# Kernel tuning notes

Hardware: AMD Instinct MI355X
Metric: run time of the kernel (lower is better)

The kernel has to match this reference:

```python
import jax, jax.numpy as jnp
import numpy as np
from jax import lax

EPS = 1e-5

def _conv(x, w, pad):
    # x: NCHW, w: OIHW, stride 1
    return lax.conv_general_dilated(x, w, (1, 1), [(pad, pad), (pad, pad)],
                                    dimension_numbers=('NCHW', 'OIHW', 'NCHW'))

def _binconv(x, w):
    # IR-Net/ReActNet HardBinaryConv: sign-binarized weights scaled by per-filter
    # mean |w| (alpha), sign-binarized activations; clip-based STE for backward.
    alpha = jnp.mean(jnp.abs(w), axis=(1, 2, 3), keepdims=True)  # [O,1,1,1]
    wc = jnp.clip(w, -1.0, 1.0)
    bw = lax.stop_gradient(alpha * jnp.sign(w) - wc) + wc
    xc = jnp.clip(x, -1.0, 1.0)
    ba = lax.stop_gradient(jnp.sign(x) - xc) + xc
    return _conv(ba, bw, 1)

def _bn(x, g, b, m, v):
    # inference-mode BatchNorm2d with running stats
    inv = g / jnp.sqrt(v + EPS)
    return x * inv[None, :, None, None] + (b - m * inv)[None, :, None, None]

def _pool(x):
    return lax.reduce_window(x, -jnp.inf, lax.max, (1, 1, 2, 2), (1, 1, 2, 2), 'VALID')

def _htanh(x):
    return jnp.clip(x, -1.0, 1.0)

def setup_inputs() -> dict:
    key = jax.random.key(0)
    ks = jax.random.split(key, 40)
    B = 256
    d = {'x': jax.random.normal(ks[0], (B, 3, 32, 32), jnp.float32)}
    shapes = [(128, 3, 3, 3), (128, 128, 3, 3), (256, 128, 3, 3),
              (256, 256, 3, 3), (512, 256, 3, 3), (512, 512, 3, 3)]
    chans = [128, 128, 256, 256, 512, 512]
    ki = 1
    for i, (ws, c) in enumerate(zip(shapes, chans)):
        fan_in = ws[1] * 9
        d[f'w{i}'] = jax.random.normal(ks[ki], ws, jnp.float32) / np.sqrt(fan_in); ki += 1
        d[f'g{i}'] = jnp.ones((c,), jnp.float32)
        d[f'b{i}'] = jnp.zeros((c,), jnp.float32)
        d[f'm{i}'] = jax.random.normal(ks[ki], (c,), jnp.float32) * 0.1; ki += 1
        d[f'v{i}'] = jax.random.uniform(ks[ki], (c,), jnp.float32, 0.5, 1.5); ki += 1
    d['fcw'] = jax.random.normal(ks[ki], (10, 512 * 4 * 4), jnp.float32) * 0.01
    d['fcb'] = jnp.zeros((10,), jnp.float32)
    return d

def reference(x, w0, g0, b0, m0, v0, w1, g1, b1, m1, v1, w2, g2, b2, m2, v2,
              w3, g3, b3, m3, v3, w4, g4, b4, m4, v4, w5, g5, b5, m5, v5,
              fcw, fcb):
    h = _bn(_conv(x, w0, 1), g0, b0, m0, v0)            # [B,128,32,32]
    h = _htanh(_bn(_pool(_binconv(h, w1)), g1, b1, m1, v1))   # [B,128,16,16]
    h = _htanh(_bn(_binconv(h, w2), g2, b2, m2, v2))          # [B,256,16,16]
    h = _htanh(_bn(_pool(_binconv(h, w3)), g3, b3, m3, v3))   # [B,256,8,8]
    h = _htanh(_bn(_binconv(h, w4), g4, b4, m4, v4))          # [B,512,8,8]
    h = _htanh(_bn(_pool(_binconv(h, w5)), g5, b5, m5, v5))   # [B,512,4,4]
    h = h.reshape(h.shape[0], -1)                             # [B,8192]
    return h @ fcw.T + fcb                                    # [B,10]
```

## Files before the change

### kernel.cpp

```cpp
#include <hip/hip_runtime.h>
#include <cstdint>

#define EPS 1e-5
typedef unsigned long long u64;
typedef unsigned int u32;

struct BnArgs { const float *g[6], *b[6], *m[6], *v[6]; };
struct PackArgs { const float* w[5]; u64* wbt[5]; };

__global__ void bn_prep_all(BnArgs p, double* __restrict__ scale_all,
                            double* __restrict__ shift_all) {
    int i = blockIdx.x * 256 + threadIdx.x;
    if (i >= 1792) return;
    int l, base;
    if (i < 128)       { l = 0; base = 0; }
    else if (i < 256)  { l = 1; base = 128; }
    else if (i < 512)  { l = 2; base = 256; }
    else if (i < 768)  { l = 3; base = 512; }
    else if (i < 1280) { l = 4; base = 768; }
    else               { l = 5; base = 1280; }
    const int c = i - base;
    double inv = (double)p.g[l][c] / sqrt((double)p.v[l][c] + EPS);
    scale_all[i] = inv;
    shift_all[i] = (double)p.b[l][c] - (double)p.m[l][c] * inv;
}

__global__ void zero_out(float* __restrict__ out, int n) {
    int i = blockIdx.x * blockDim.x + threadIdx.x;
    if (i < n) out[i] = 0.f;
}

__global__ void pack_all(PackArgs pk, const double* __restrict__ scale_all,
                         double* __restrict__ A_all) {
    const int ob = blockIdx.x;
    const int t = threadIdx.x;
    int l, base, Cin, bnoff, OTOT;
    if (ob < 128)       { l = 0; base = 0;    Cin = 128; bnoff = 128;  OTOT = 128; }
    else if (ob < 384)  { l = 1; base = 128;  Cin = 128; bnoff = 256;  OTOT = 256; }
    else if (ob < 640)  { l = 2; base = 384;  Cin = 256; bnoff = 512;  OTOT = 256; }
    else if (ob < 1152) { l = 3; base = 640;  Cin = 256; bnoff = 768;  OTOT = 512; }
    else                { l = 4; base = 1152; Cin = 512; bnoff = 1280; OTOT = 512; }
    const int o = ob - base;
    const float* wo = pk.w[l] + (size_t)o * Cin * 9;

    double s = 0.0;
    for (int k = t; k < Cin * 9; k += 256) s += fabs((double)wo[k]);
    __shared__ double red[256];
    red[t] = s;
    __syncthreads();
    for (int r = 128; r > 0; r >>= 1) {
        if (t < r) red[t] += red[t + r];
        __syncthreads();
    }
    if (t == 0) {
        double alpha = red[0] / (double)(Cin * 9);
        A_all[ob] = alpha * scale_all[bnoff + o];
    }

    const int W64 = Cin / 64;
    u64* wbt = pk.wbt[l];
    for (int e = t; e < 9 * W64; e += 256) {
        int tap = e / W64, word = e % W64;
        u64 bits = 0;
        for (int j = 0; j < 64; ++j) {
            int c = word * 64 + j;
            if (wo[c * 9 + tap] < 0.f) bits |= (1ull << j);
        }
        wbt[((size_t)tap * OTOT + o) * W64 + word] = bits;
    }
}

__global__ __launch_bounds__(256) void conv0_pack(
        const float* __restrict__ x, const float* __restrict__ w0,
        const double* __restrict__ scale, const double* __restrict__ shift,
        u64* __restrict__ bits0) {
    __shared__ double wlds[128 * 27];
    __shared__ double sc[128], sh[128];
    const int tid = threadIdx.x;
    for (int e = tid; e < 128 * 27; e += 256) wlds[e] = (double)w0[e];
    for (int e = tid; e < 128; e += 256) { sc[e] = scale[e]; sh[e] = shift[e]; }
    __syncthreads();

    const int n = blockIdx.y;
    const int p = blockIdx.x * 256 + tid;
    const int y = p >> 5, xx = p & 31;
    const float* xn = x + (size_t)n * 3 * 32 * 32;

    double win[27];
#pragma unroll
    for (int c = 0; c < 3; ++c)
#pragma unroll
        for (int dy = 0; dy < 3; ++dy)
#pragma unroll
            for (int dx = 0; dx < 3; ++dx) {
                const int yy = y + dy - 1, xs = xx + dx - 1;
                const bool ok = (yy >= 0 && yy < 32 && xs >= 0 && xs < 32);
                win[(c * 3 + dy) * 3 + dx] = ok ? (double)xn[(c * 32 + yy) * 32 + xs] : 0.0;
            }

    u64* op = bits0 + ((size_t)n * 1024 + p) * 2;
#pragma unroll
    for (int og = 0; og < 2; ++og) {
        u64 word = 0;
#pragma unroll 2
        for (int j = 0; j < 64; ++j) {
            const int o = og * 64 + j;
            const double* wo = &wlds[o * 27];
            double acc = 0.0;
#pragma unroll
            for (int k = 0; k < 27; ++k) acc = fma(wo[k], win[k], acc);
            const double val = acc * sc[o] + sh[o];
            word |= (u64)(val < 0.0) << j;
        }
        op[og] = word;
    }
}

template<int H, int W, int W64, int OTOT, bool POOL, bool LAST, int MINW>
__global__ __launch_bounds__(256, MINW) void bconv4(
        const u64* __restrict__ in_bits, const u64* __restrict__ wbt,
        const double* __restrict__ A, const double* __restrict__ B,
        u32* __restrict__ out_bits, float* __restrict__ h5) {
    const int tid = threadIdx.x;
    const int wave = tid >> 6, lane = tid & 63;
    constexpr int OPW = 32;
    constexpr int WPI = (H * W) / 64;
    constexpr int IPB = (WPI >= 4) ? 1 : (4 / WPI);
    const int img = (IPB == 1) ? blockIdx.z : blockIdx.z * IPB + wave;
    const int wii = (IPB == 1) ? (blockIdx.y * 4 + wave) : 0;
    const int y = wii * (64 / W) + lane / W;
    const int x = lane % W;
    const int obase = blockIdx.x * OPW;

    __shared__ u64 wl[9 * OPW * W64];
    __shared__ double Ald[OPW], Bld[OPW];
    {
        for (int e = tid; e < 9 * OPW * W64; e += 256) {
            const int tap = e / (OPW * W64), r = e % (OPW * W64);
            wl[e] = wbt[((size_t)tap * OTOT + obase) * W64 + r];
        }
        for (int e = tid; e < OPW; e += 256) {
            Ald[e] = A[obase + e];
            Bld[e] = B[obase + e];
        }
    }
    __syncthreads();

    const u64* ib = in_bits + (size_t)img * H * W * W64;

    int acc[OPW];
#pragma unroll
    for (int i = 0; i < OPW; ++i) acc[i] = 0;
    int nvalid = 0;

#pragma unroll 1
    for (int dy = 0; dy < 3; ++dy) {
#pragma unroll 1
        for (int dx = 0; dx < 3; ++dx) {
            const int yy = y + dy - 1, xs = x + dx - 1;
            const bool ok = (yy >= 0 && yy < H && xs >= 0 && xs < W);
            nvalid += ok ? 1 : 0;
            u64 wn[W64];
            const u64* q = ib + ((size_t)yy * W + xs) * W64;
#pragma unroll
            for (int k = 0; k < W64; ++k) wn[k] = ok ? q[k] : 0ull;
            const u64* wt = &wl[(dy * 3 + dx) * OPW * W64];
#pragma unroll
            for (int oc = 0; oc < OPW; ++oc) {
                int tp = 0;
#pragma unroll
                for (int k = 0; k < W64; ++k)
                    tp += (int)__popcll(wn[k] ^ wt[oc * W64 + k]);
                acc[oc] += ok ? tp : 0;
            }
        }
    }

    const int basev = nvalid * 64 * W64;
    constexpr int Hp = POOL ? H / 2 : H, Wp = POOL ? W / 2 : W;
    const bool writer = (!POOL) || (((lane & 1) == 0) && ((lane & W) == 0));
    const int py = POOL ? (y >> 1) : y, px = POOL ? (x >> 1) : x;

    u32 cur = 0;
#pragma unroll
    for (int oc = 0; oc < OPW; ++oc) {
        int v = basev - 2 * acc[oc];
        if (POOL) {
            int v2 = max(v, __shfl_xor(v, 1, 64));
            v = max(v2, __shfl_xor(v2, W, 64));
        }
        const double t = fma(Ald[oc], (double)v, Bld[oc]);
        if (LAST) {
            const double hcl = fmin(1.0, fmax(-1.0, t));
            if (writer)
                h5[(((size_t)img * OTOT + obase + oc) * Hp + py) * Wp + px] = (float)hcl;
        } else {
            cur |= (u32)(t < 0.0) << oc;
        }
    }
    if (!LAST && writer) {
        out_bits[((size_t)img * Hp * Wp + (size_t)py * Wp + px) * (OTOT / 32) + (obase >> 5)] = cur;
    }
}

__global__ void fc_kernel(const float* __restrict__ h, const float* __restrict__ fcw,
                          const float* __restrict__ fcb, float* __restrict__ out) {
    const int n = blockIdx.x, t = threadIdx.x;
    double acc[10];
#pragma unroll
    for (int j = 0; j < 10; ++j) acc[j] = 0.0;
    const float* hn = h + (size_t)n * 8192;
    for (int k = t; k < 8192; k += 256) {
        double xv = (double)hn[k];
#pragma unroll
        for (int j = 0; j < 10; ++j) acc[j] += xv * (double)fcw[j * 8192 + k];
    }
    __shared__ double red[10][256];
#pragma unroll
    for (int j = 0; j < 10; ++j) red[j][t] = acc[j];
    __syncthreads();
    for (int r = 128; r > 0; r >>= 1) {
        if (t < r) {
#pragma unroll
            for (int j = 0; j < 10; ++j) red[j][t] += red[j][t + r];
        }
        __syncthreads();
    }
    if (t < 10) out[n * 10 + t] = (float)(red[t][0] + (double)fcb[t]);
}

extern "C" void kernel_launch(void* const* d_in, const int* in_sizes, int n_in,
                              void* d_out, int out_size, void* d_ws, size_t ws_size,
                              hipStream_t stream) {
    const float* X = (const float*)d_in[0];
    BnArgs bn;
    PackArgs pk;
    const float* Wt0 = (const float*)d_in[1];
    for (int i = 0; i < 6; ++i) {
        bn.g[i] = (const float*)d_in[2 + 5 * i];
        bn.b[i] = (const float*)d_in[3 + 5 * i];
        bn.m[i] = (const float*)d_in[4 + 5 * i];
        bn.v[i] = (const float*)d_in[5 + 5 * i];
    }
    for (int i = 0; i < 5; ++i) pk.w[i] = (const float*)d_in[1 + 5 * (i + 1)];
    const float* fcw = (const float*)d_in[31];
    const float* fcb = (const float*)d_in[32];
    float* out = (float*)d_out;

    char* ws = (char*)d_ws;
    size_t off = 0;
    auto alloc = [&](size_t bytes) -> void* {
        void* p = ws + off;
        off = (off + bytes + 255) & ~(size_t)255;
        return p;
    };

    double* scale_all = (double*)alloc(1792 * sizeof(double));
    double* shift_all = (double*)alloc(1792 * sizeof(double));
    double* A_all     = (double*)alloc(1664 * sizeof(double));
    const size_t WBN[5] = {128ull * 9 * 2, 256ull * 9 * 2, 256ull * 9 * 4,
                           512ull * 9 * 4, 512ull * 9 * 8};
    for (int i = 0; i < 5; ++i) pk.wbt[i] = (u64*)alloc(WBN[i] * sizeof(u64));
    u64* bits0 = (u64*)alloc(256ull * 32 * 32 * 2 * sizeof(u64));
    u64* bits1 = (u64*)alloc(256ull * 16 * 16 * 2 * sizeof(u64));
    u64* bits2 = (u64*)alloc(256ull * 16 * 16 * 4 * sizeof(u64));
    u64* bits3 = (u64*)alloc(256ull * 8 * 8 * 4 * sizeof(u64));
    u64* bits4 = (u64*)alloc(256ull * 8 * 8 * 8 * sizeof(u64));
    float* h5  = (float*)alloc(256ull * 8192 * sizeof(float));

    if (off > ws_size) {
        zero_out<<<dim3((out_size + 255) / 256), dim3(256), 0, stream>>>(out, out_size);
        return;
    }

    const int BOF[6] = {0, 128, 256, 512, 768, 1280};
    const int AOF[5] = {0, 128, 384, 640, 1152};

    bn_prep_all<<<dim3(7), dim3(256), 0, stream>>>(bn, scale_all, shift_all);
    pack_all<<<dim3(1664), dim3(256), 0, stream>>>(pk, scale_all, A_all);

    conv0_pack<<<dim3(4, 256), dim3(256), 0, stream>>>(
        X, Wt0, scale_all + BOF[0], shift_all + BOF[0], bits0);

    bconv4<32, 32, 2, 128, true, false, 4><<<dim3(4, 4, 256), dim3(256), 0, stream>>>(
        bits0, pk.wbt[0], A_all + AOF[0], shift_all + BOF[1], (u32*)bits1, nullptr);
    bconv4<16, 16, 2, 256, false, false, 4><<<dim3(8, 1, 256), dim3(256), 0, stream>>>(
        bits1, pk.wbt[1], A_all + AOF[1], shift_all + BOF[2], (u32*)bits2, nullptr);
    bconv4<16, 16, 4, 256, true, false, 4><<<dim3(8, 1, 256), dim3(256), 0, stream>>>(
        bits2, pk.wbt[2], A_all + AOF[2], shift_all + BOF[3], (u32*)bits3, nullptr);
    bconv4<8, 8, 4, 512, false, false, 4><<<dim3(16, 1, 64), dim3(256), 0, stream>>>(
        bits3, pk.wbt[3], A_all + AOF[3], shift_all + BOF[4], (u32*)bits4, nullptr);
    bconv4<8, 8, 8, 512, true, true, 4><<<dim3(16, 1, 64), dim3(256), 0, stream>>>(
        bits4, pk.wbt[4], A_all + AOF[4], shift_all + BOF[5], nullptr, h5);

    fc_kernel<<<dim3(256), dim3(256), 0, stream>>>(h5, fcw, fcb, out);
}
```

Measured before the change: 588.4 us.

## Pad bit activation buffers with zero halos and precompute border-correction table

Activation bit buffers now carry a one-pixel zero border, so the binary conv inner loop loads neighbours without bounds checks or per-tap masking. Zero-padded taps XOR to the weight bits, so a per-block table indexed by border pattern precomputes the valid-count minus the spurious weight popcounts. This removes branches and selects from the popcount loop. In exchange there is an extra zeroing kernel over all bit buffers each call, slightly larger buffers, and h5 now aliases the bit buffers.

```diff
diff --git a/kernel.cpp b/kernel.cpp
--- a/kernel.cpp
+++ b/kernel.cpp
@@ -30,6 +30,12 @@
     if (i < n) out[i] = 0.f;
 }
 
+__global__ void zero_u64(u64* __restrict__ p, size_t n) {
+    size_t i = (size_t)blockIdx.x * 256 + threadIdx.x;
+    const size_t step = (size_t)gridDim.x * 256;
+    for (; i < n; i += step) p[i] = 0ull;
+}
+
 __global__ void pack_all(PackArgs pk, const double* __restrict__ scale_all,
                          double* __restrict__ A_all) {
     const int ob = blockIdx.x;
@@ -98,7 +104,7 @@
                 win[(c * 3 + dy) * 3 + dx] = ok ? (double)xn[(c * 32 + yy) * 32 + xs] : 0.0;
             }
 
-    u64* op = bits0 + ((size_t)n * 1024 + p) * 2;
+    u64* op = bits0 + (((size_t)n * 34 + (y + 1)) * 34 + (xx + 1)) * 2;
 #pragma unroll
     for (int og = 0; og < 2; ++og) {
         u64 word = 0;
@@ -117,7 +123,7 @@
 }
 
 template<int H, int W, int W64, int OTOT, bool POOL, bool LAST, int MINW>
-__global__ __launch_bounds__(256, MINW) void bconv4(
+__global__ __launch_bounds__(256, MINW) void bconv5(
         const u64* __restrict__ in_bits, const u64* __restrict__ wbt,
         const double* __restrict__ A, const double* __restrict__ B,
         u32* __restrict__ out_bits, float* __restrict__ h5) {
@@ -133,6 +139,7 @@
     const int obase = blockIdx.x * OPW;
 
     __shared__ u64 wl[9 * OPW * W64];
+    __shared__ u32 ct[16 * OPW];
     __shared__ double Ald[OPW], Bld[OPW];
     {
         for (int e = tid; e < 9 * OPW * W64; e += 256) {
@@ -145,38 +152,54 @@
         }
     }
     __syncthreads();
-
-    const u64* ib = in_bits + (size_t)img * H * W * W64;
+    for (int e = tid; e < 16 * OPW; e += 256) {
+        const int pat = e >> 5, oc = e & 31;
+        int nv = 0;
+        u32 cor = 0;
+#pragma unroll
+        for (int tap = 0; tap < 9; ++tap) {
+            const int dy = tap / 3, dx = tap % 3;
+            const bool inv = ((pat & 1) && dy == 0) || ((pat & 2) && dy == 2) ||
+                             ((pat & 4) && dx == 0) || ((pat & 8) && dx == 2);
+            if (inv) {
+#pragma unroll
+                for (int k = 0; k < W64; ++k)
+                    cor += (u32)__popcll(wl[(tap * OPW + oc) * W64 + k]);
+            } else {
+                nv++;
+            }
+        }
+        ct[e] = (u32)(nv * 64 * W64) + 2u * cor;
+    }
+    __syncthreads();
+
+    constexpr int RC = W + 2;
+    const u64* ib = in_bits + (size_t)img * (H + 2) * RC * W64;
 
     int acc[OPW];
 #pragma unroll
     for (int i = 0; i < OPW; ++i) acc[i] = 0;
-    int nvalid = 0;
 
 #pragma unroll 1
     for (int dy = 0; dy < 3; ++dy) {
 #pragma unroll 1
         for (int dx = 0; dx < 3; ++dx) {
-            const int yy = y + dy - 1, xs = x + dx - 1;
-            const bool ok = (yy >= 0 && yy < H && xs >= 0 && xs < W);
-            nvalid += ok ? 1 : 0;
+            const u64* q = ib + ((size_t)(y + dy) * RC + (x + dx)) * W64;
             u64 wn[W64];
-            const u64* q = ib + ((size_t)yy * W + xs) * W64;
-#pragma unroll
-            for (int k = 0; k < W64; ++k) wn[k] = ok ? q[k] : 0ull;
+#pragma unroll
+            for (int k = 0; k < W64; ++k) wn[k] = q[k];
             const u64* wt = &wl[(dy * 3 + dx) * OPW * W64];
 #pragma unroll
             for (int oc = 0; oc < OPW; ++oc) {
-                int tp = 0;
 #pragma unroll
                 for (int k = 0; k < W64; ++k)
-                    tp += (int)__popcll(wn[k] ^ wt[oc * W64 + k]);
-                acc[oc] += ok ? tp : 0;
+                    acc[oc] += (int)__popcll(wn[k] ^ wt[oc * W64 + k]);
             }
         }
     }
 
-    const int basev = nvalid * 64 * W64;
+    const int pat = (y == 0 ? 1 : 0) | (y == H - 1 ? 2 : 0) |
+                    (x == 0 ? 4 : 0) | (x == W - 1 ? 8 : 0);
     constexpr int Hp = POOL ? H / 2 : H, Wp = POOL ? W / 2 : W;
     const bool writer = (!POOL) || (((lane & 1) == 0) && ((lane & W) == 0));
     const int py = POOL ? (y >> 1) : y, px = POOL ? (x >> 1) : x;
@@ -184,7 +207,7 @@
     u32 cur = 0;
 #pragma unroll
     for (int oc = 0; oc < OPW; ++oc) {
-        int v = basev - 2 * acc[oc];
+        int v = (int)ct[(pat << 5) | oc] - 2 * acc[oc];
         if (POOL) {
             int v2 = max(v, __shfl_xor(v, 1, 64));
             v = max(v2, __shfl_xor(v2, W, 64));
@@ -199,7 +222,8 @@
         }
     }
     if (!LAST && writer) {
-        out_bits[((size_t)img * Hp * Wp + (size_t)py * Wp + px) * (OTOT / 32) + (obase >> 5)] = cur;
+        out_bits[(((size_t)img * (Hp + 2) + (py + 1)) * (Wp + 2) + (px + 1)) * (OTOT / 32)
+                 + (obase >> 5)] = cur;
     }
 }
 
@@ -261,12 +285,19 @@
     const size_t WBN[5] = {128ull * 9 * 2, 256ull * 9 * 2, 256ull * 9 * 4,
                            512ull * 9 * 4, 512ull * 9 * 8};
     for (int i = 0; i < 5; ++i) pk.wbt[i] = (u64*)alloc(WBN[i] * sizeof(u64));
-    u64* bits0 = (u64*)alloc(256ull * 32 * 32 * 2 * sizeof(u64));
-    u64* bits1 = (u64*)alloc(256ull * 16 * 16 * 2 * sizeof(u64));
-    u64* bits2 = (u64*)alloc(256ull * 16 * 16 * 4 * sizeof(u64));
-    u64* bits3 = (u64*)alloc(256ull * 8 * 8 * 4 * sizeof(u64));
-    u64* bits4 = (u64*)alloc(256ull * 8 * 8 * 8 * sizeof(u64));
-    float* h5  = (float*)alloc(256ull * 8192 * sizeof(float));
+    u64* bits4 = (u64*)alloc(256ull * 10 * 10 * 8 * sizeof(u64));
+    u64* bits0 = (u64*)alloc(256ull * 34 * 34 * 2 * sizeof(u64));
+    u64* bits1 = (u64*)alloc(256ull * 18 * 18 * 2 * sizeof(u64));
+    u64* bits2 = (u64*)alloc(256ull * 18 * 18 * 4 * sizeof(u64));
+    u64* bits3 = (u64*)alloc(256ull * 10 * 10 * 4 * sizeof(u64));
+    const size_t bits_u64 =
+        256ull * (10 * 10 * 8 + 34 * 34 * 2 + 18 * 18 * 2 + 18 * 18 * 4 + 10 * 10 * 4);
+    float* h5 = (float*)bits0;
+    {
+        const size_t h5_bytes = 256ull * 8192 * sizeof(float);
+        const size_t have = (size_t)((char*)(bits3 + 256ull * 10 * 10 * 4) - (char*)bits0);
+        if (h5_bytes > have) alloc(h5_bytes - have);
+    }
 
     if (off > ws_size) {
         zero_out<<<dim3((out_size + 255) / 256), dim3(256), 0, stream>>>(out, out_size);
@@ -278,19 +309,20 @@
 
     bn_prep_all<<<dim3(7), dim3(256), 0, stream>>>(bn, scale_all, shift_all);
     pack_all<<<dim3(1664), dim3(256), 0, stream>>>(pk, scale_all, A_all);
+    zero_u64<<<dim3(2048), dim3(256), 0, stream>>>(bits4, bits_u64);
 
     conv0_pack<<<dim3(4, 256), dim3(256), 0, stream>>>(
         X, Wt0, scale_all + BOF[0], shift_all + BOF[0], bits0);
 
-    bconv4<32, 32, 2, 128, true, false, 4><<<dim3(4, 4, 256), dim3(256), 0, stream>>>(
+    bconv5<32, 32, 2, 128, true, false, 4><<<dim3(4, 4, 256), dim3(256), 0, stream>>>(
         bits0, pk.wbt[0], A_all + AOF[0], shift_all + BOF[1], (u32*)bits1, nullptr);
-    bconv4<16, 16, 2, 256, false, false, 4><<<dim3(8, 1, 256), dim3(256), 0, stream>>>(
+    bconv5<16, 16, 2, 256, false, false, 4><<<dim3(8, 1, 256), dim3(256), 0, stream>>>(
         bits1, pk.wbt[1], A_all + AOF[1], shift_all + BOF[2], (u32*)bits2, nullptr);
-    bconv4<16, 16, 4, 256, true, false, 4><<<dim3(8, 1, 256), dim3(256), 0, stream>>>(
+    bconv5<16, 16, 4, 256, true, false, 4><<<dim3(8, 1, 256), dim3(256), 0, stream>>>(
         bits2, pk.wbt[2], A_all + AOF[2], shift_all + BOF[3], (u32*)bits3, nullptr);
-    bconv4<8, 8, 4, 512, false, false, 4><<<dim3(16, 1, 64), dim3(256), 0, stream>>>(
+    bconv5<8, 8, 4, 512, false, false, 4><<<dim3(16, 1, 64), dim3(256), 0, stream>>>(
         bits3, pk.wbt[3], A_all + AOF[3], shift_all + BOF[4], (u32*)bits4, nullptr);
-    bconv4<8, 8, 8, 512, true, true, 4><<<dim3(16, 1, 64), dim3(256), 0, stream>>>(
+    bconv5<8, 8, 8, 512, true, true, 4><<<dim3(16, 1, 64), dim3(256), 0, stream>>>(
         bits4, pk.wbt[4], A_all + AOF[4], shift_all + BOF[5], nullptr, h5);
 
     fc_kernel<<<dim3(256), dim3(256), 0, stream>>>(h5, fcw, fcb, out);
```

After: 601.2 us. +2.2%, slower.
